# Performance work log

Measured on AMD Instinct MI355X. Metric: run time of the kernel, lower is better.

The kernel has to match this reference:

```python
import jax, jax.numpy as jnp
import numpy as np

# Model constants (match init_kwargs config)
D_MODEL, D_INNER, D_HEAD, N_HEADS = 1024, 2048, 64, 32
D_STATE, D_CONV, CHUNK, N_LAYERS = 64, 4, 256, 2
CONV_DIM = D_INNER + 2 * D_STATE        # n_groups = 1
D_IN_PROJ = 2 * D_INNER + 2 * D_STATE + N_HEADS
B_SZ, L_SEQ = 2, 4096
EPS = 1e-5


def setup_inputs() -> dict:
    key = jax.random.key(0)
    ks = jax.random.split(key, 8)
    x = jax.random.normal(ks[0], (B_SZ, L_SEQ, D_MODEL), jnp.float32)
    in_proj_w = jax.random.normal(ks[1], (N_LAYERS, D_IN_PROJ, D_MODEL), jnp.float32) * 0.02
    conv_w = jax.random.normal(ks[2], (N_LAYERS, CONV_DIM, D_CONV), jnp.float32) * 0.2
    conv_b = jax.random.normal(ks[3], (N_LAYERS, CONV_DIM), jnp.float32) * 0.02
    # dt_bias init as in the torch code: inverse-softplus of dt ~ LogUniform(1e-3, 1e-1)
    dt = jnp.exp(jax.random.uniform(ks[4], (N_LAYERS, N_HEADS))
                 * (np.log(0.1) - np.log(0.001)) + np.log(0.001))
    dt = jnp.clip(dt, 1e-4, None)
    dt_bias = dt + jnp.log(-jnp.expm1(-dt))
    A_log = jnp.log(jax.random.uniform(ks[5], (N_LAYERS, N_HEADS), minval=1.0, maxval=16.0))
    D = jnp.ones((N_LAYERS, N_HEADS), jnp.float32)
    gnorm_w = jnp.ones((N_LAYERS, D_INNER), jnp.float32)
    out_proj_w = jax.random.normal(ks[6], (N_LAYERS, D_MODEL, D_INNER), jnp.float32) * 0.02
    norm_w = jnp.ones((N_LAYERS, D_MODEL), jnp.float32)
    return dict(x=x, in_proj_w=in_proj_w, conv_w=conv_w, conv_b=conv_b, dt_bias=dt_bias,
                A_log=A_log, D=D, gnorm_w=gnorm_w, out_proj_w=out_proj_w, norm_w=norm_w)


def _rmsnorm(x, w, eps=EPS):
    return x * jax.lax.rsqrt(jnp.mean(x * x, axis=-1, keepdims=True) + eps) * w


def _segsum(x):
    # x: (..., T) -> (..., T, T) with S[i, j] = sum_{j < k <= i} x[k], -inf above diag
    T = x.shape[-1]
    cs = jnp.cumsum(x, axis=-1)
    d = cs[..., :, None] - cs[..., None, :]
    return jnp.where(jnp.tril(jnp.ones((T, T), bool)), d, -jnp.inf)


def _causal_conv1d(x, w, b):
    # depthwise causal conv: x (B,L,C), w (C,K), b (C)
    K = w.shape[-1]
    L = x.shape[1]
    xp = jnp.pad(x, ((0, 0), (K - 1, 0), (0, 0)))
    out = jnp.broadcast_to(b, x.shape)
    for i in range(K):
        out = out + xp[:, i:i + L, :] * w[:, i]
    return out


def _ssd(X, dt, A, B, C, D):
    # Exact chunked SSD scan (mamba_chunk_scan_combined), n_groups=1.
    # X (b,l,h,p), dt (b,l,h), A (h), B,C (b,l,n)
    b, l, h, p = X.shape
    n = B.shape[-1]
    nc = l // CHUNK
    Xdt = X * dt[..., None]
    dA = (dt * A).reshape(b, nc, CHUNK, h).transpose(0, 3, 1, 2)     # (b,h,z,c)
    dAcs = jnp.cumsum(dA, axis=-1)
    Lmat = jnp.exp(_segsum(dA))                                      # (b,h,z,c,c)
    Bc = B.reshape(b, nc, CHUNK, n)
    Cc = C.reshape(b, nc, CHUNK, n)
    Xc = Xdt.reshape(b, nc, CHUNK, h, p)
    # intra-chunk (diagonal) part
    G = jnp.einsum('bzln,bzsn->bzls', Cc, Bc)                        # (b,z,c,c)
    M = G[:, None] * Lmat                                            # (b,h,z,c,c)
    Yd = jnp.einsum('bhzls,bzshp->bzlhp', M, Xc)
    # chunk states
    decay_states = jnp.exp(dAcs[..., -1:] - dAcs)                    # (b,h,z,c)
    states = jnp.einsum('bzln,bhzl,bzlhp->bzhpn', Bc, decay_states, Xc)
    # inter-chunk recurrence
    chunk_decay = jnp.exp(_segsum(jnp.pad(dAcs[..., -1], ((0, 0), (0, 0), (1, 0)))))
    states0 = jnp.concatenate([jnp.zeros_like(states[:, :1]), states], axis=1)
    prev = jnp.einsum('bhzc,bchpn->bzhpn', chunk_decay, states0)[:, :-1]
    Yo = jnp.einsum('bzln,bzhpn,bhzl->bzlhp', Cc, prev, jnp.exp(dAcs))
    Y = (Yd + Yo).reshape(b, l, h, p) + X * D[None, None, :, None]
    return Y


def _block(x, in_w, cw, cb, dtb, a_log, d_skip, gw, ow, nw):
    b, l, _ = x.shape
    h = _rmsnorm(x, nw)
    zxbcdt = jnp.einsum('bld,ed->ble', h, in_w)
    z = zxbcdt[..., :D_INNER]
    xBC = zxbcdt[..., D_INNER:D_INNER + CONV_DIM]
    dt = jax.nn.softplus(zxbcdt[..., D_INNER + CONV_DIM:] + dtb)      # (b,l,H)
    xBC = jax.nn.silu(_causal_conv1d(xBC, cw, cb))
    xs = xBC[..., :D_INNER].reshape(b, l, N_HEADS, D_HEAD)
    Bm = xBC[..., D_INNER:D_INNER + D_STATE]
    Cm = xBC[..., D_INNER + D_STATE:]
    A = -jnp.exp(a_log)
    y = _ssd(xs, dt, A, Bm, Cm, d_skip).reshape(b, l, D_INNER)
    y = _rmsnorm(y * jax.nn.silu(z), gw)                              # gated RMSNorm (gate before norm)
    return x + jnp.einsum('bli,di->bld', y, ow)


def reference(x, in_proj_w, conv_w, conv_b, dt_bias, A_log, D, gnorm_w, out_proj_w, norm_w):
    for i in range(in_proj_w.shape[0]):
        x = _block(x, in_proj_w[i], conv_w[i], conv_b[i], dt_bias[i],
                   A_log[i], D[i], gnorm_w[i], out_proj_w[i], norm_w[i])
    return x
```

## Files before the change

### kernel.cpp

```cpp
#include <hip/hip_runtime.h>

#define DMODEL   1024
#define DINNER   2048
#define NHEADS   32
#define DHEAD    64
#define DSTATE   64
#define CONVDIM  2176
#define DINPROJ  4256
#define LSEQ     4096
#define BSZ      2
#define NCHUNK   16
#define CHUNK    256
#define NROWS    8192
#define NPAD     4352
#define XT_P     264
#define M_P      40

typedef __attribute__((ext_vector_type(8))) short  short8;
typedef __attribute__((ext_vector_type(4))) float  f32x4;
typedef __attribute__((ext_vector_type(4))) unsigned short us4;

__device__ __forceinline__ float bf2f(unsigned short u){
  return __uint_as_float(((unsigned int)u) << 16);
}
__device__ __forceinline__ unsigned short f2bf(float f){
  unsigned int i = __float_as_uint(f);
  i += 0x7fffu + ((i >> 16) & 1u);
  return (unsigned short)(i >> 16);
}

__device__ __forceinline__ void gl_lds16(const void* g, void* l){
  __builtin_amdgcn_global_load_lds(
      (const __attribute__((address_space(1))) unsigned int*)g,
      (__attribute__((address_space(3))) unsigned int*)l, 16, 0, 0);
}

__global__ void cast_pad_kernel(const float* __restrict__ src, unsigned short* __restrict__ dst,
                                int rows_src, int cols, long long total){
  long long i = (long long)blockIdx.x * 256 + threadIdx.x;
  if (i >= total) return;
  long long r = i / cols;
  dst[i] = (r < rows_src) ? f2bf(src[i]) : (unsigned short)0;
}

__global__ void rmsnorm_kernel(const float* __restrict__ x, const float* __restrict__ w,
                               unsigned short* __restrict__ out){
  int r = blockIdx.x, t = threadIdx.x;
  const float* xr = x + (size_t)r * DMODEL;
  float v[4]; float s = 0.f;
#pragma unroll
  for (int i = 0; i < 4; ++i){ v[i] = xr[t + i*256]; s += v[i]*v[i]; }
  __shared__ float red[4];
  for (int off = 32; off; off >>= 1) s += __shfl_down(s, off, 64);
  if ((t & 63) == 0) red[t >> 6] = s;
  __syncthreads();
  s = red[0] + red[1] + red[2] + red[3];
  float sc = rsqrtf(s * (1.f/DMODEL) + 1e-5f);
#pragma unroll
  for (int i = 0; i < 4; ++i)
    out[(size_t)r*DMODEL + t + i*256] = f2bf(v[i]*sc*w[t + i*256]);
}

template<int EPI>
__launch_bounds__(256, 3)
__global__ void gemm_bt(const unsigned short* __restrict__ A, const unsigned short* __restrict__ Bw,
                        void* __restrict__ Cout, const float* __restrict__ Cres,
                        int K, int Nstore){
  __shared__ __align__(16) unsigned short As[128*64];
  __shared__ __align__(16) unsigned short Bs[128*64];
  const int m0 = blockIdx.y * 128, n0 = blockIdx.x * 128;
  const int t = threadIdx.x, w = t >> 6, lane = t & 63;
  const int wr = w >> 1, wc = w & 1;
  const int srow = lane >> 3;
  const int scol = (lane & 7) * 8;
  f32x4 acc[4][4] = {};

  for (int k0 = 0; k0 < K; k0 += 64){
#pragma unroll
    for (int it = 0; it < 4; ++it){
      int rr = (w*4 + it)*8 + srow;
      gl_lds16(A  + (size_t)(m0 + rr)*K + k0 + scol, &As[(w*4 + it)*512]);
      gl_lds16(Bw + (size_t)(n0 + rr)*K + k0 + scol, &Bs[(w*4 + it)*512]);
    }
    __syncthreads();
#pragma unroll
    for (int kk = 0; kk < 64; kk += 32){
      short8 af[4], bfr[4];
      int col = kk + (lane >> 4)*8;
#pragma unroll
      for (int m = 0; m < 4; ++m)
        af[m] = *(const short8*)&As[(wr*64 + m*16 + (lane & 15))*64 + col];
#pragma unroll
      for (int n = 0; n < 4; ++n)
        bfr[n] = *(const short8*)&Bs[(wc*64 + n*16 + (lane & 15))*64 + col];
#pragma unroll
      for (int m = 0; m < 4; ++m)
#pragma unroll
        for (int n = 0; n < 4; ++n)
          acc[m][n] = __builtin_amdgcn_mfma_f32_16x16x32_bf16(af[m], bfr[n], acc[m][n], 0, 0, 0);
    }
    __syncthreads();
  }

#pragma unroll
  for (int m = 0; m < 4; ++m){
#pragma unroll
    for (int n = 0; n < 4; ++n){
      int col = n0 + wc*64 + n*16 + (lane & 15);
      if (col < Nstore){
#pragma unroll
        for (int r = 0; r < 4; ++r){
          int row = m0 + wr*64 + m*16 + (lane >> 4)*4 + r;
          if (EPI == 0)
            ((unsigned short*)Cout)[(size_t)row*Nstore + col] = f2bf(acc[m][n][r]);
          else
            ((float*)Cout)[(size_t)row*Nstore + col] =
                Cres[(size_t)row*Nstore + col] + acc[m][n][r];
        }
      }
    }
  }
}

__global__ void conv_silu_kernel(const unsigned short* __restrict__ zx,
                                 const float* __restrict__ cw, const float* __restrict__ cb,
                                 unsigned short* __restrict__ X, unsigned short* __restrict__ Bm,
                                 unsigned short* __restrict__ Cm){
  int c = blockIdx.x * 256 + threadIdx.x;
  if (c >= CONVDIM) return;
  int r = blockIdx.y;
  int l = r & (LSEQ - 1);
  float acc = cb[c];
  float w0 = cw[c*4+0], w1 = cw[c*4+1], w2 = cw[c*4+2], w3 = cw[c*4+3];
#pragma unroll
  for (int i = 0; i < 4; ++i){
    int li = l - 3 + i;
    if (li >= 0){
      float v = bf2f(zx[(size_t)(r - 3 + i)*DINPROJ + DINNER + c]);
      float wi = (i==0)?w0:(i==1)?w1:(i==2)?w2:w3;
      acc += v * wi;
    }
  }
  float s = acc / (1.f + __expf(-acc));
  if (c < DINNER)            X[(size_t)r*DINNER + c]        = f2bf(s);
  else if (c < DINNER+DSTATE) Bm[(size_t)r*DSTATE + c-DINNER] = f2bf(s);
  else                        Cm[(size_t)r*DSTATE + c-DINNER-DSTATE] = f2bf(s);
}

__global__ void dtscan_kernel(const unsigned short* __restrict__ zx, const float* __restrict__ dtb,
                              const float* __restrict__ A_log,
                              float* __restrict__ dt_sp, float* __restrict__ dAcs_g){
  const int z = blockIdx.x, hh = blockIdx.y, b = blockIdx.z;
  const int t = threadIdx.x;
  __shared__ float sdA[CHUNK];
  const float Ah = -__expf(A_log[hh]);
  size_t r = (size_t)b*LSEQ + z*CHUNK + t;
  float raw = bf2f(zx[r*DINPROJ + DINNER + CONVDIM + hh]) + dtb[hh];
  float dtv = raw > 20.f ? raw : log1pf(__expf(raw));
  sdA[t] = dtv * Ah;
  __syncthreads();
  for (int off = 1; off < CHUNK; off <<= 1){
    float v = (t >= off) ? sdA[t - off] : 0.f;
    __syncthreads();
    sdA[t] += v;
    __syncthreads();
  }
  size_t hb = (size_t)(b*NHEADS + hh);
  dt_sp[hb*LSEQ + z*CHUNK + t] = dtv;
  dAcs_g[(hb*NCHUNK + z)*CHUNK + t] = sdA[t];
}

__launch_bounds__(256, 2)
__global__ void chunk_main_kernel(const unsigned short* __restrict__ X,
                                  const unsigned short* __restrict__ Bm,
                                  const unsigned short* __restrict__ Cm,
                                  const float* __restrict__ dt_sp,
                                  const float* __restrict__ dAcs_g,
                                  float* __restrict__ states,
                                  unsigned short* __restrict__ Yb){
  const int z = blockIdx.x, hh = blockIdx.y, b = blockIdx.z;
  const int t = threadIdx.x, w = t >> 6, lane = t & 63;
  __shared__ __align__(16) unsigned short Xt[64 * XT_P];
  __shared__ __align__(16) unsigned short U[64 * XT_P];
  __shared__ float sdA[CHUNK];
  __shared__ float sdt[CHUNK];

  const size_t row0 = (size_t)b*LSEQ + z*CHUNK;
  const size_t hb = (size_t)(b*NHEADS + hh);
  sdA[t] = dAcs_g[(hb*NCHUNK + z)*CHUNK + t];
  sdt[t] = dt_sp[hb*LSEQ + z*CHUNK + t];
  __syncthreads();
  const float total = sdA[CHUNK-1];

  for (int it = 0; it < 16; ++it){
    int l = it*16 + (t >> 4);
    int p4 = (t & 15) * 4;
    float dtl = sdt[l];
    float dec = __expf(total - sdA[l]);
    us4 xv = *(const us4*)(X  + (row0 + l)*DINNER + hh*DHEAD + p4);
    us4 bv = *(const us4*)(Bm + (row0 + l)*DSTATE + p4);
#pragma unroll
    for (int j = 0; j < 4; ++j){
      Xt[(p4 + j)*XT_P + l] = f2bf(bf2f(xv[j]) * dtl);
      U [(p4 + j)*XT_P + l] = f2bf(bf2f(bv[j]) * dec);
    }
  }
  __syncthreads();

  {
    f32x4 sacc[4] = {};
    for (int k2 = 0; k2 < 8; ++k2){
      int kc = k2*32 + (lane >> 4)*8;
      short8 a = *(const short8*)&U[(w*16 + (lane & 15))*XT_P + kc];
#pragma unroll
      for (int pt = 0; pt < 4; ++pt){
        short8 bfr = *(const short8*)&Xt[(pt*16 + (lane & 15))*XT_P + kc];
        sacc[pt] = __builtin_amdgcn_mfma_f32_16x16x32_bf16(a, bfr, sacc[pt], 0, 0, 0);
      }
    }
    float* sp = states + (((size_t)b*NCHUNK + z)*NHEADS + hh)*(DHEAD*DSTATE);
#pragma unroll
    for (int pt = 0; pt < 4; ++pt){
      int p = pt*16 + (lane & 15);
#pragma unroll
      for (int r = 0; r < 4; ++r){
        int n = w*16 + (lane >> 4)*4 + r;
        sp[p*DSTATE + n] = sacc[pt][r];
      }
    }
  }
  __syncthreads();

  unsigned short* Mw = U + w * (64 * M_P);
  short8 cfr[4][2];
#pragma unroll
  for (int lt = 0; lt < 4; ++lt){
    int lg = w + lt*4;
#pragma unroll
    for (int k2 = 0; k2 < 2; ++k2)
      cfr[lt][k2] = *(const short8*)(Cm + (row0 + lg*16 + (lane & 15))*DSTATE + k2*32 + (lane >> 4)*8);
  }
  f32x4 yacc[4][4] = {};
  for (int st = 0; st < 8; ++st){
    short8 gb[2][2];
#pragma unroll
    for (int ss = 0; ss < 2; ++ss)
#pragma unroll
      for (int k2 = 0; k2 < 2; ++k2)
        gb[ss][k2] = *(const short8*)(Bm + (row0 + st*32 + ss*16 + (lane & 15))*DSTATE + k2*32 + (lane >> 4)*8);
    short8 xb[4];
#pragma unroll
    for (int pt = 0; pt < 4; ++pt)
      xb[pt] = *(const short8*)&Xt[(pt*16 + (lane & 15))*XT_P + st*32 + (lane >> 4)*8];
#pragma unroll
    for (int lt = 0; lt < 4; ++lt){
      int lg = w + lt*4;
      if (st*32 > lg*16 + 15) continue;
#pragma unroll
      for (int ss = 0; ss < 2; ++ss){
        f32x4 g = {};
        g = __builtin_amdgcn_mfma_f32_16x16x32_bf16(cfr[lt][0], gb[ss][0], g, 0, 0, 0);
        g = __builtin_amdgcn_mfma_f32_16x16x32_bf16(cfr[lt][1], gb[ss][1], g, 0, 0, 0);
        int s = st*32 + ss*16 + (lane & 15);
        float sdAs = sdA[s];
#pragma unroll
        for (int r = 0; r < 4; ++r){
          int l = lg*16 + (lane >> 4)*4 + r;
          float m = (s <= l) ? __expf(sdA[l] - sdAs) : 0.f;
          Mw[(lt*16 + (lane >> 4)*4 + r)*M_P + ss*16 + (lane & 15)] = f2bf(g[r] * m);
        }
      }
      short8 mf = *(const short8*)&Mw[(lt*16 + (lane & 15))*M_P + (lane >> 4)*8];
#pragma unroll
      for (int pt = 0; pt < 4; ++pt)
        yacc[lt][pt] = __builtin_amdgcn_mfma_f32_16x16x32_bf16(mf, xb[pt], yacc[lt][pt], 0, 0, 0);
    }
  }
  __syncthreads();

  unsigned short* Yst = U + w * 4096;
#pragma unroll
  for (int lt = 0; lt < 4; ++lt)
#pragma unroll
    for (int pt = 0; pt < 4; ++pt)
#pragma unroll
      for (int r = 0; r < 4; ++r){
        int row = lt*16 + (lane >> 4)*4 + r;
        int c = pt*16 + (lane & 15);
        int cs = (c & 7) | ((((c >> 3) ^ (row & 7)) & 7) << 3);
        Yst[row*64 + cs] = f2bf(yacc[lt][pt][r]);
      }
  __syncthreads();
  {
    int ltl = lane >> 4, rr = lane & 15;
    int row = ltl*16 + rr;
    int lg = (w + ltl*4)*16 + rr;
    unsigned short* dst = Yb + (row0 + lg)*DINNER + hh*DHEAD;
#pragma unroll
    for (int k = 0; k < 8; ++k){
      short8 v = *(const short8*)&Yst[row*64 + ((k ^ (row & 7)) << 3)];
      *(short8*)(dst + k*8) = v;
    }
  }
}

__launch_bounds__(256)
__global__ void state_recur_kernel(const float* __restrict__ states, const float* __restrict__ dAcs_g,
                                   unsigned short* __restrict__ prev_bf){
  const int hh = blockIdx.x, b = blockIdx.y, t = threadIdx.x;
  float S[16];
#pragma unroll
  for (int k = 0; k < 16; ++k) S[k] = 0.f;
  for (int z = 0; z < NCHUNK; ++z){
    size_t base = (((size_t)b*NCHUNK + z)*NHEADS + hh)*(DHEAD*DSTATE);
    float cd = __expf(dAcs_g[(((size_t)(b*NHEADS + hh))*NCHUNK + z)*CHUNK + CHUNK-1]);
#pragma unroll
    for (int k = 0; k < 16; ++k){
      size_t idx = base + (size_t)k*256 + t;
      float st = states[idx];
      prev_bf[idx] = f2bf(S[k]);
      S[k] = S[k]*cd + st;
    }
  }
}

__launch_bounds__(256, 2)
__global__ void chunk_out_kernel(const unsigned short* __restrict__ X,
                                 const unsigned short* __restrict__ Cm,
                                 const float* __restrict__ dAcs_g, const unsigned short* __restrict__ prev_bf,
                                 const float* __restrict__ Dp, unsigned short* __restrict__ Yb){
  const int z = blockIdx.x, hh = blockIdx.y, b = blockIdx.z;
  const int t = threadIdx.x, w = t >> 6, lane = t & 63;
  __shared__ __align__(16) float Yo[4][64*64];
  __shared__ float sdA[CHUNK];
  const size_t row0 = (size_t)b*LSEQ + z*CHUNK;
  sdA[t] = dAcs_g[(((size_t)(b*NHEADS + hh))*NCHUNK + z)*CHUNK + t];
  __syncthreads();
  const unsigned short* pvb = prev_bf + (((size_t)b*NCHUNK + z)*NHEADS + hh)*(DHEAD*DSTATE);
  const float Dh = Dp[hh];

  f32x4 acc[4][4] = {};
#pragma unroll
  for (int k2 = 0; k2 < 2; ++k2){
    int kc = k2*32 + (lane >> 4)*8;
    short8 a[4], bfr[4];
#pragma unroll
    for (int lt = 0; lt < 4; ++lt)
      a[lt] = *(const short8*)(Cm + (row0 + w*64 + lt*16 + (lane & 15))*DSTATE + kc);
#pragma unroll
    for (int pt = 0; pt < 4; ++pt)
      bfr[pt] = *(const short8*)(pvb + (size_t)(pt*16 + (lane & 15))*DSTATE + kc);
#pragma unroll
    for (int lt = 0; lt < 4; ++lt)
#pragma unroll
      for (int pt = 0; pt < 4; ++pt)
        acc[lt][pt] = __builtin_amdgcn_mfma_f32_16x16x32_bf16(a[lt], bfr[pt], acc[lt][pt], 0, 0, 0);
  }

#pragma unroll
  for (int lt = 0; lt < 4; ++lt){
    float eA[4];
#pragma unroll
    for (int r = 0; r < 4; ++r)
      eA[r] = __expf(sdA[w*64 + lt*16 + (lane >> 4)*4 + r]);
#pragma unroll
    for (int pt = 0; pt < 4; ++pt){
      int c = pt*16 + (lane & 15);
#pragma unroll
      for (int r = 0; r < 4; ++r){
        int row = lt*16 + (lane >> 4)*4 + r;
        int blk = ((c >> 2) ^ (row & 15)) & 15;
        Yo[w][row*64 + (c & 3) + (blk << 2)] = acc[lt][pt][r] * eA[r];
      }
    }
  }
  __syncthreads();
  {
    int l = w*64 + lane;
    const unsigned short* xr = X + (row0 + l)*DINNER + hh*DHEAD;
    unsigned short* yr = Yb + (row0 + l)*DINNER + hh*DHEAD;
#pragma unroll
    for (int k = 0; k < 16; ++k){
      f32x4 v = *(const f32x4*)&Yo[w][lane*64 + (((k ^ (lane & 15)) & 15) << 2)];
      us4 yb = *(const us4*)(yr + k*4);
      us4 xv = *(const us4*)(xr + k*4);
      us4 o;
#pragma unroll
      for (int j = 0; j < 4; ++j)
        o[j] = f2bf(bf2f(yb[j]) + v[j] + Dh*bf2f(xv[j]));
      *(us4*)(yr + k*4) = o;
    }
  }
}

__global__ void gated_rmsnorm_kernel(const unsigned short* __restrict__ Yb,
                                     const unsigned short* __restrict__ zx,
                                     const float* __restrict__ gw, unsigned short* __restrict__ out){
  int r = blockIdx.x, t = threadIdx.x;
  float vals[8]; float s = 0.f;
#pragma unroll
  for (int i = 0; i < 8; ++i){
    int c = t + i*256;
    float y  = bf2f(Yb[(size_t)r*DINNER + c]);
    float zv = bf2f(zx[(size_t)r*DINPROJ + c]);
    float g  = y * (zv / (1.f + __expf(-zv)));
    vals[i] = g; s += g*g;
  }
  __shared__ float red[4];
  for (int off = 32; off; off >>= 1) s += __shfl_down(s, off, 64);
  if ((t & 63) == 0) red[t >> 6] = s;
  __syncthreads();
  s = red[0] + red[1] + red[2] + red[3];
  float sc = rsqrtf(s * (1.f/DINNER) + 1e-5f);
#pragma unroll
  for (int i = 0; i < 8; ++i)
    out[(size_t)r*DINNER + t + i*256] = f2bf(vals[i]*sc*gw[t + i*256]);
}

extern "C" void kernel_launch(void* const* d_in, const int* in_sizes, int n_in,
                              void* d_out, int out_size, void* d_ws, size_t ws_size,
                              hipStream_t stream){
  const float* x      = (const float*)d_in[0];
  const float* in_w   = (const float*)d_in[1];
  const float* conv_w = (const float*)d_in[2];
  const float* conv_b = (const float*)d_in[3];
  const float* dt_b   = (const float*)d_in[4];
  const float* A_log  = (const float*)d_in[5];
  const float* Dp     = (const float*)d_in[6];
  const float* gnw    = (const float*)d_in[7];
  const float* out_w  = (const float*)d_in[8];
  const float* norm_w = (const float*)d_in[9];
  float* outp = (float*)d_out;

  const size_t NEEDED =
      (size_t)NROWS*DMODEL*2 + (size_t)NPAD*DMODEL*2 + (size_t)DMODEL*DINNER*2
    + (size_t)NROWS*DINPROJ*2 + (size_t)NROWS*DINNER*2  + (size_t)NROWS*DINNER*2
    + (size_t)NROWS*DSTATE*2*2 + (size_t)BSZ*NHEADS*LSEQ*4
    + (size_t)BSZ*NHEADS*NCHUNK*CHUNK*4
    + (size_t)BSZ*NCHUNK*NHEADS*DHEAD*DSTATE*4
    + (size_t)BSZ*NCHUNK*NHEADS*DHEAD*DSTATE*2
    + 40*256;
  if (ws_size < NEEDED) return;

  char* p = (char*)d_ws;
  auto alloc = [&](size_t n){ char* r = p; p += (n + 255) & ~(size_t)255; return (void*)r; };
  unsigned short* h    = (unsigned short*)alloc((size_t)NROWS*DMODEL*2);
  unsigned short* wA   = (unsigned short*)alloc((size_t)NPAD*DMODEL*2);
  unsigned short* wO   = (unsigned short*)alloc((size_t)DMODEL*DINNER*2);
  unsigned short* zx   = (unsigned short*)alloc((size_t)NROWS*DINPROJ*2);
  unsigned short* X    = (unsigned short*)alloc((size_t)NROWS*DINNER*2);
  unsigned short* Yb   = (unsigned short*)alloc((size_t)NROWS*DINNER*2);
  unsigned short* Bm   = (unsigned short*)alloc((size_t)NROWS*DSTATE*2);
  unsigned short* Cm   = (unsigned short*)alloc((size_t)NROWS*DSTATE*2);
  float* dtbuf  = (float*)alloc((size_t)BSZ*NHEADS*LSEQ*4);
  float* dAcs   = (float*)alloc((size_t)BSZ*NHEADS*NCHUNK*CHUNK*4);
  float* states = (float*)alloc((size_t)BSZ*NCHUNK*NHEADS*DHEAD*DSTATE*4);
  unsigned short* prev_bf = (unsigned short*)alloc((size_t)BSZ*NCHUNK*NHEADS*DHEAD*DSTATE*2);
  unsigned short* yn = X;

  for (int layer = 0; layer < 2; ++layer){
    const float* xprev = (layer == 0) ? x : outp;
    float* xnext = outp;

    cast_pad_kernel<<<(NPAD*DMODEL + 255)/256, 256, 0, stream>>>(
        in_w + (size_t)layer*DINPROJ*DMODEL, wA, DINPROJ, DMODEL, (long long)NPAD*DMODEL);
    rmsnorm_kernel<<<NROWS, 256, 0, stream>>>(xprev, norm_w + layer*DMODEL, h);
    gemm_bt<0><<<dim3(NPAD/128, NROWS/128), 256, 0, stream>>>(
        h, wA, (void*)zx, nullptr, DMODEL, DINPROJ);
    conv_silu_kernel<<<dim3((CONVDIM + 255)/256, NROWS), 256, 0, stream>>>(
        zx, conv_w + (size_t)layer*CONVDIM*4, conv_b + layer*CONVDIM, X, Bm, Cm);
    dtscan_kernel<<<dim3(NCHUNK, NHEADS, BSZ), 256, 0, stream>>>(
        zx, dt_b + layer*NHEADS, A_log + layer*NHEADS, dtbuf, dAcs);
    chunk_main_kernel<<<dim3(NCHUNK, NHEADS, BSZ), 256, 0, stream>>>(
        X, Bm, Cm, dtbuf, dAcs, states, Yb);
    state_recur_kernel<<<dim3(NHEADS, BSZ), 256, 0, stream>>>(states, dAcs, prev_bf);
    chunk_out_kernel<<<dim3(NCHUNK, NHEADS, BSZ), 256, 0, stream>>>(
        X, Cm, dAcs, prev_bf, Dp + layer*NHEADS, Yb);
    gated_rmsnorm_kernel<<<NROWS, 256, 0, stream>>>(Yb, zx, gnw + layer*DINNER, yn);
    cast_pad_kernel<<<(DMODEL*DINNER + 255)/256, 256, 0, stream>>>(
        out_w + (size_t)layer*DMODEL*DINNER, wO, DMODEL, DINNER, (long long)DMODEL*DINNER);
    gemm_bt<1><<<dim3(DMODEL/128, NROWS/128), 256, 0, stream>>>(
        yn, wO, (void*)xnext, xprev, DINNER, DMODEL);
  }
  (void)in_sizes; (void)n_in; (void)out_size;
}
```

Measured before the change: 764.4 us.

## Vectorize conv with sliding-window rows and store chunk_out staging in bf16

The causal conv kernel now has each thread handle 8 contiguous channels over 64 consecutive rows. It uses 16-byte vector loads and stores and keeps a register sliding window, so each input row is read once instead of four times. In chunk_out, the shared-memory staging buffer for the off-diagonal output drops from fp32 to bf16 and the occupancy hint rises from 2 to 4 blocks. That halves LDS use to allow more resident blocks, at the cost of an extra bf16 rounding of the intermediate before the final add.

```diff
diff --git a/kernel.cpp b/kernel.cpp
--- a/kernel.cpp
+++ b/kernel.cpp
@@ -126,25 +126,51 @@
                                  const float* __restrict__ cw, const float* __restrict__ cb,
                                  unsigned short* __restrict__ X, unsigned short* __restrict__ Bm,
                                  unsigned short* __restrict__ Cm){
-  int c = blockIdx.x * 256 + threadIdx.x;
-  if (c >= CONVDIM) return;
-  int r = blockIdx.y;
-  int l = r & (LSEQ - 1);
-  float acc = cb[c];
-  float w0 = cw[c*4+0], w1 = cw[c*4+1], w2 = cw[c*4+2], w3 = cw[c*4+3];
-#pragma unroll
-  for (int i = 0; i < 4; ++i){
-    int li = l - 3 + i;
-    if (li >= 0){
-      float v = bf2f(zx[(size_t)(r - 3 + i)*DINPROJ + DINNER + c]);
-      float wi = (i==0)?w0:(i==1)?w1:(i==2)?w2:w3;
-      acc += v * wi;
-    }
-  }
-  float s = acc / (1.f + __expf(-acc));
-  if (c < DINNER)            X[(size_t)r*DINNER + c]        = f2bf(s);
-  else if (c < DINNER+DSTATE) Bm[(size_t)r*DSTATE + c-DINNER] = f2bf(s);
-  else                        Cm[(size_t)r*DSTATE + c-DINNER-DSTATE] = f2bf(s);
+  int gid = blockIdx.x*256 + threadIdx.x;
+  if (gid >= (CONVDIM/8)*(NROWS/64)) return;
+  const int oc = gid % (CONVDIM/8);
+  const int rb = gid / (CONVDIM/8);
+  const int c = oc*8;
+  const size_t r0 = (size_t)rb*64;
+  const int l0 = (int)(r0 & (LSEQ-1));
+  float w[4][8], bias[8];
+#pragma unroll
+  for (int j = 0; j < 8; ++j){
+    bias[j] = cb[c+j];
+#pragma unroll
+    for (int i = 0; i < 4; ++i) w[i][j] = cw[(c+j)*4 + i];
+  }
+  const unsigned short* src = zx + DINNER + c;
+  float p[3][8];
+#pragma unroll
+  for (int i = 0; i < 3; ++i){
+    if (l0 - 3 + i >= 0){
+      short8 v = *(const short8*)(src + (r0 - 3 + i)*DINPROJ);
+#pragma unroll
+      for (int j = 0; j < 8; ++j) p[i][j] = bf2f((unsigned short)v[j]);
+    } else {
+#pragma unroll
+      for (int j = 0; j < 8; ++j) p[i][j] = 0.f;
+    }
+  }
+  for (int it = 0; it < 64; ++it){
+    const size_t r = r0 + it;
+    short8 v = *(const short8*)(src + r*DINPROJ);
+    float cur[8];
+    short8 ov;
+#pragma unroll
+    for (int j = 0; j < 8; ++j){
+      cur[j] = bf2f((unsigned short)v[j]);
+      float a = bias[j] + w[0][j]*p[0][j] + w[1][j]*p[1][j] + w[2][j]*p[2][j] + w[3][j]*cur[j];
+      float s = a / (1.f + __expf(-a));
+      ov[j] = (short)f2bf(s);
+    }
+    if (c < DINNER)             *(short8*)(X  + r*DINNER + c) = ov;
+    else if (c < DINNER+DSTATE) *(short8*)(Bm + r*DSTATE + (c-DINNER)) = ov;
+    else                        *(short8*)(Cm + r*DSTATE + (c-DINNER-DSTATE)) = ov;
+#pragma unroll
+    for (int j = 0; j < 8; ++j){ p[0][j]=p[1][j]; p[1][j]=p[2][j]; p[2][j]=cur[j]; }
+  }
 }
 
 __global__ void dtscan_kernel(const unsigned short* __restrict__ zx, const float* __restrict__ dtb,
@@ -324,14 +350,14 @@
   }
 }
 
-__launch_bounds__(256, 2)
+__launch_bounds__(256, 4)
 __global__ void chunk_out_kernel(const unsigned short* __restrict__ X,
                                  const unsigned short* __restrict__ Cm,
                                  const float* __restrict__ dAcs_g, const unsigned short* __restrict__ prev_bf,
                                  const float* __restrict__ Dp, unsigned short* __restrict__ Yb){
   const int z = blockIdx.x, hh = blockIdx.y, b = blockIdx.z;
   const int t = threadIdx.x, w = t >> 6, lane = t & 63;
-  __shared__ __align__(16) float Yo[4][64*64];
+  __shared__ __align__(16) unsigned short Yo[4][64*64];
   __shared__ float sdA[CHUNK];
   const size_t row0 = (size_t)b*LSEQ + z*CHUNK;
   sdA[t] = dAcs_g[(((size_t)(b*NHEADS + hh))*NCHUNK + z)*CHUNK + t];
@@ -370,7 +396,7 @@
       for (int r = 0; r < 4; ++r){
         int row = lt*16 + (lane >> 4)*4 + r;
         int blk = ((c >> 2) ^ (row & 15)) & 15;
-        Yo[w][row*64 + (c & 3) + (blk << 2)] = acc[lt][pt][r] * eA[r];
+        Yo[w][row*64 + (c & 3) + (blk << 2)] = f2bf(acc[lt][pt][r] * eA[r]);
       }
     }
   }
@@ -381,13 +407,13 @@
     unsigned short* yr = Yb + (row0 + l)*DINNER + hh*DHEAD;
 #pragma unroll
     for (int k = 0; k < 16; ++k){
-      f32x4 v = *(const f32x4*)&Yo[w][lane*64 + (((k ^ (lane & 15)) & 15) << 2)];
+      us4 v = *(const us4*)&Yo[w][lane*64 + (((k ^ (lane & 15)) & 15) << 2)];
       us4 yb = *(const us4*)(yr + k*4);
       us4 xv = *(const us4*)(xr + k*4);
       us4 o;
 #pragma unroll
       for (int j = 0; j < 4; ++j)
-        o[j] = f2bf(bf2f(yb[j]) + v[j] + Dh*bf2f(xv[j]));
+        o[j] = f2bf(bf2f(yb[j]) + bf2f(v[j]) + Dh*bf2f(xv[j]));
       *(us4*)(yr + k*4) = o;
     }
   }
@@ -467,7 +493,7 @@
     rmsnorm_kernel<<<NROWS, 256, 0, stream>>>(xprev, norm_w + layer*DMODEL, h);
     gemm_bt<0><<<dim3(NPAD/128, NROWS/128), 256, 0, stream>>>(
         h, wA, (void*)zx, nullptr, DMODEL, DINPROJ);
-    conv_silu_kernel<<<dim3((CONVDIM + 255)/256, NROWS), 256, 0, stream>>>(
+    conv_silu_kernel<<<((CONVDIM/8)*(NROWS/64) + 255)/256, 256, 0, stream>>>(
         zx, conv_w + (size_t)layer*CONVDIM*4, conv_b + layer*CONVDIM, X, Bm, Cm);
     dtscan_kernel<<<dim3(NCHUNK, NHEADS, BSZ), 256, 0, stream>>>(
         zx, dt_b + layer*NHEADS, A_log + layer*NHEADS, dtbuf, dAcs);
```

New measurement: 732.6 us. 1.04x faster.
